# Performance work log

Measured on AMD Instinct MI355X. Metric: run time of the kernel, lower is better.

## Reference

```python
import jax, jax.numpy as jnp
import numpy as np


def setup_inputs() -> dict:
    key = jax.random.key(0)
    kq, kk, kv, km = jax.random.split(key, 4)
    B, H, S, D = 2, 16, 2048, 64
    Q = jax.random.normal(kq, (B, H, S, D), dtype=jnp.float32)
    K = jax.random.normal(kk, (B, H, S, D), dtype=jnp.float32)
    V = jax.random.normal(kv, (B, H, S, D), dtype=jnp.float32)
    mask = jax.random.randint(km, (B, 1, S, S), 0, 2).astype(jnp.bool_)
    return {"Q": Q, "K": K, "V": V, "mask": mask}


def reference(Q, K, V, mask):
    # scores: [B, H, Sq, Sk]
    scores = jnp.einsum("bhqd,bhkd->bhqk", Q, K)
    neg = jnp.finfo(scores.dtype).min
    # Faithful to original: mask fill happens BEFORE the sqrt(d) scaling.
    scores = jnp.where(mask, neg, scores)
    inv_sqrt_d = 1.0 / jnp.sqrt(jnp.asarray(Q.shape[-1], dtype=scores.dtype))
    attn = jax.nn.softmax(scores * inv_sqrt_d, axis=-1)
    return jnp.einsum("bhqk,bhkd->bhqd", attn, V)
```

## Files before the change

kernel.cpp:

```cpp
#include <hip/hip_runtime.h>
#include <stdint.h>


#define SQ 2048
#define DH 64

using bf16x8  = __attribute__((ext_vector_type(8)))  __bf16;
using f32x4   = __attribute__((ext_vector_type(4)))  float;
using ushort8 = __attribute__((ext_vector_type(8)))  unsigned short;
using ushort4v= __attribute__((ext_vector_type(4)))  unsigned short;
using u32x4   = __attribute__((ext_vector_type(4)))  unsigned int;

static __device__ __forceinline__ unsigned short f2bf(float f) {
    union { float f; uint32_t u; } c; c.f = f;
    return (unsigned short)((c.u + 0x8000u) >> 16);
}

static __device__ __forceinline__ uint32_t pkbf(float a, float b) {
    union { __bf16 h[2]; uint32_t u; } t;
    t.h[0] = (__bf16)a; t.h[1] = (__bf16)b;
    return t.u;
}

static __device__ __forceinline__ f32x4 mfma16(bf16x8 a, bf16x8 b, f32x4 c) {
    return __builtin_amdgcn_mfma_f32_16x16x32_bf16(a, b, c, 0, 0, 0);
}

static __device__ __forceinline__ void gload16(const void* g, void* l) {
    __builtin_amdgcn_global_load_lds(
        (const __attribute__((address_space(1))) void*)g,
        (__attribute__((address_space(3))) void*)l, 16, 0, 0);
}

__global__ __launch_bounds__(256)
void prep_kernel(const int* __restrict__ mask, const float* __restrict__ K,
                 const float* __restrict__ V, unsigned long long* __restrict__ words,
                 unsigned short* __restrict__ Kb, unsigned short* __restrict__ Vt) {
    __shared__ unsigned short tl[64][66];
    const int bx  = blockIdx.x;
    const int tid = threadIdx.x;
    if (bx < 32768) {
        int gid = bx * 256 + tid;
        int mv = mask[gid];
        unsigned long long b = __ballot(mv != 0);
        if ((gid & 63) == 0) words[gid >> 6] = b;
    } else if (bx < 36864) {
        int gid = (bx - 32768) * 256 + tid;
        float4 v = ((const float4*)K)[gid];
        ushort4v t;
        t[0]=f2bf(v.x); t[1]=f2bf(v.y); t[2]=f2bf(v.z); t[3]=f2bf(v.w);
        ((ushort4v*)Kb)[gid] = t;
    } else {
        const int vbx = bx - 36864;
        const int kt  = vbx & 31;
        const size_t bh = vbx >> 5;
        const float* vp = V + (bh * SQ + (size_t)kt * 64) * DH;
        #pragma unroll
        for (int i = 0; i < 4; ++i) {
            int idx = tid + 256 * i;
            int key = idx >> 4;
            int dc  = (idx & 15) * 4;
            float4 v = *(const float4*)(vp + (size_t)key * DH + dc);
            tl[key][dc + 0] = f2bf(v.x);
            tl[key][dc + 1] = f2bf(v.y);
            tl[key][dc + 2] = f2bf(v.z);
            tl[key][dc + 3] = f2bf(v.w);
        }
        __syncthreads();
        unsigned short* op = Vt + bh * DH * SQ + (size_t)kt * 64;
        #pragma unroll
        for (int i = 0; i < 4; ++i) {
            int idx = tid + 256 * i;
            int d  = idx >> 4;
            int kc = (idx & 15) * 4;
            ushort4v t;
            t[0] = tl[kc + 0][d]; t[1] = tl[kc + 1][d];
            t[2] = tl[kc + 2][d]; t[3] = tl[kc + 3][d];
            *(ushort4v*)(op + (size_t)d * SQ + kc) = t;
        }
    }
}

__global__ __launch_bounds__(256, 5)
void attn_kernel(const float* __restrict__ Q,
                 const unsigned short* __restrict__ Kb,
                 const unsigned short* __restrict__ Vtg,
                 const unsigned long long* __restrict__ Mw,
                 float* __restrict__ out) {
    __shared__ __align__(16) unsigned short Ks[2][64 * 64];
    __shared__ __align__(16) unsigned short Vs[2][64 * 64];

    const int tid  = threadIdx.x;
    const int w    = tid >> 6;
    const int l    = tid & 63;
    const int quad = l >> 4;
    const int c16  = l & 15;
    const int bx = blockIdx.x;
    const int hh = bx & 15;
    const int b  = (bx >> 4) & 1;
    const int qt = bx >> 5;

    const size_t bh = (size_t)b * 16 + hh;
    const float* Qp = Q + bh * SQ * DH;
    const int qw = qt * 64 + 16 * w;

    const unsigned long long* Mrow = Mw + ((size_t)b * SQ + qw + c16) * (SQ / 64);

    const int s0 = (2 * w) * 64 + l;
    const int s1 = (2 * w + 1) * 64 + l;
    const int r0 = s0 >> 3, g0s = s0 & 7;
    const int r1 = s1 >> 3, g1s = s1 & 7;
    const char* Kg = (const char*)(Kb  + bh * (size_t)SQ * DH);
    const char* Vg = (const char*)(Vtg + bh * (size_t)DH * SQ);
    const char* kSrc0 = Kg + r0 * 128  + ((g0s ^ (r0 & 7)) << 4);
    const char* kSrc1 = Kg + r1 * 128  + ((g1s ^ (r1 & 7)) << 4);
    const char* vSrc0 = Vg + r0 * 4096 + ((g0s ^ (r0 & 7)) << 4);
    const char* vSrc1 = Vg + r1 * 4096 + ((g1s ^ (r1 & 7)) << 4);

    bf16x8 qf[2];
    {
        const float* qr = Qp + (size_t)(qw + c16) * DH;
        #pragma unroll
        for (int c = 0; c < 2; ++c) {
            int d0 = 32 * c + 8 * quad;
            float4 a  = *(const float4*)(qr + d0);
            float4 b4 = *(const float4*)(qr + d0 + 4);
            ushort8 t;
            t[0]=f2bf(a.x);  t[1]=f2bf(a.y);  t[2]=f2bf(a.z);  t[3]=f2bf(a.w);
            t[4]=f2bf(b4.x); t[5]=f2bf(b4.y); t[6]=f2bf(b4.z); t[7]=f2bf(b4.w);
            qf[c] = __builtin_bit_cast(bf16x8, t);
        }
    }

    f32x4 o[4];
    float lsum = 0.f;
    #pragma unroll
    for (int i = 0; i < 4; ++i) o[i] = (f32x4)(0.f);

    const int xg = (c16 & 7);
    int gfrag[2];
    #pragma unroll
    for (int c = 0; c < 2; ++c) gfrag[c] = ((4 * c + quad) ^ xg) << 3;

    const int permA = ((quad & 1) << 1) | (quad >> 1);
    const int addrA = 4 * (c16 + 16 * permA);
    const int addrB = addrA ^ 64;
    const bool oddq = (quad & 1) != 0;

    unsigned long long mw = Mrow[0];

    gload16(kSrc0, &Ks[0][(2 * w) * 512]);
    gload16(kSrc1, &Ks[0][(2 * w + 1) * 512]);
    gload16(vSrc0, &Vs[0][(2 * w) * 512]);
    gload16(vSrc1, &Vs[0][(2 * w + 1) * 512]);
    kSrc0 += 8192; kSrc1 += 8192; vSrc0 += 128; vSrc1 += 128;
    __syncthreads();

    for (int t = 0; t < 32; ++t) {
        const int cur = t & 1;

        unsigned long long nmw = 0;
        if (t < 31) {
            gload16(kSrc0, &Ks[cur ^ 1][(2 * w) * 512]);
            gload16(kSrc1, &Ks[cur ^ 1][(2 * w + 1) * 512]);
            gload16(vSrc0, &Vs[cur ^ 1][(2 * w) * 512]);
            gload16(vSrc1, &Vs[cur ^ 1][(2 * w + 1) * 512]);
            kSrc0 += 8192; kSrc1 += 8192; vSrc0 += 128; vSrc1 += 128;
            nmw = Mrow[t + 1];
        }

        const unsigned short* Kc = Ks[cur];
        const unsigned short* Vc = Vs[cur];

        f32x4 s[4];
        #pragma unroll
        for (int i = 0; i < 4; ++i) s[i] = (f32x4)(0.f);
        __builtin_amdgcn_s_setprio(1);
        #pragma unroll
        for (int c = 0; c < 2; ++c) {
            #pragma unroll
            for (int nb = 0; nb < 4; ++nb) {
                bf16x8 kb = __builtin_bit_cast(bf16x8,
                    *(const ushort8*)&Kc[(c16 + 16 * nb) * 64 + gfrag[c]]);
                s[nb] = mfma16(kb, qf[c], s[nb]);
            }
        }
        __builtin_amdgcn_s_setprio(0);

        const unsigned long long sh = mw >> (4 * quad);
        uint32_t pk[4][2];
        #pragma unroll
        for (int nb = 0; nb < 4; ++nb) {
            float pv[4];
            #pragma unroll
            for (int r = 0; r < 4; ++r) {
                float e = __builtin_amdgcn_exp2f(fmaf(s[nb][r], 0.18033688f, -5.7707802f));
                pv[r] = ((sh >> (16 * nb + r)) & 1ull) ? 0.0f : e;
                lsum += pv[r];
            }
            pk[nb][0] = pkbf(pv[0], pv[1]);
            pk[nb][1] = pkbf(pv[2], pv[3]);
        }

        int sw1_0 = __builtin_amdgcn_ds_swizzle((int)pk[1][0], 0x401F);
        int sw1_1 = __builtin_amdgcn_ds_swizzle((int)pk[1][1], 0x401F);
        int sw3_0 = __builtin_amdgcn_ds_swizzle((int)pk[3][0], 0x401F);
        int sw3_1 = __builtin_amdgcn_ds_swizzle((int)pk[3][1], 0x401F);

        #pragma unroll
        for (int c = 0; c < 2; ++c) {
            const int e0 = (int)pk[2 * c][0];
            const int e1 = (int)pk[2 * c][1];
            const int s0v = c ? sw3_0 : sw1_0;
            const int s1v = c ? sw3_1 : sw1_1;
            u32x4 pw;
            pw[0] = (unsigned)__builtin_amdgcn_ds_bpermute(addrA, oddq ? s0v : e0);
            pw[1] = (unsigned)__builtin_amdgcn_ds_bpermute(addrA, oddq ? s1v : e1);
            pw[2] = (unsigned)__builtin_amdgcn_ds_bpermute(addrB, oddq ? e0 : s0v);
            pw[3] = (unsigned)__builtin_amdgcn_ds_bpermute(addrB, oddq ? e1 : s1v);
            bf16x8 pa = __builtin_bit_cast(bf16x8, pw);

            __builtin_amdgcn_s_setprio(1);
            #pragma unroll
            for (int db = 0; db < 4; ++db) {
                bf16x8 vb = __builtin_bit_cast(bf16x8,
                    *(const ushort8*)&Vc[(c16 + 16 * db) * 64 + gfrag[c]]);
                o[db] = mfma16(vb, pa, o[db]);
            }
            __builtin_amdgcn_s_setprio(0);
        }

        __syncthreads();
        mw = nmw;
    }

    float v = lsum;
    v += __shfl_xor(v, 16, 64);
    v += __shfl_xor(v, 32, 64);
    const float rinv = 1.0f / v;
    float* op = out + (bh * SQ + (size_t)(qw + c16)) * DH + 4 * quad;
    #pragma unroll
    for (int db = 0; db < 4; ++db) {
        float4 st;
        st.x = o[db][0] * rinv; st.y = o[db][1] * rinv;
        st.z = o[db][2] * rinv; st.w = o[db][3] * rinv;
        *(float4*)(op + 16 * db) = st;
    }
}

extern "C" void kernel_launch(void* const* d_in, const int* in_sizes, int n_in,
                              void* d_out, int out_size, void* d_ws, size_t ws_size,
                              hipStream_t stream) {
    const float* Q    = (const float*)d_in[0];
    const float* K    = (const float*)d_in[1];
    const float* V    = (const float*)d_in[2];
    const int*   mask = (const int*)d_in[3];
    float* out = (float*)d_out;

    char* ws = (char*)d_ws;
    unsigned long long* mwords = (unsigned long long*)ws;
    unsigned short* Kb = (unsigned short*)(ws + (1 << 20));
    unsigned short* Vt = (unsigned short*)(ws + (1 << 20) + (8 << 20));

    prep_kernel<<<dim3(37888), dim3(256), 0, stream>>>(mask, K, V, mwords, Kb, Vt);
    attn_kernel<<<dim3(1024), dim3(256), 0, stream>>>(Q, Kb, Vt, mwords, out);
}
```

Baseline: 191.1 us.

## Use two-wave blocks with 32 query rows per wave and LDS P transpose

Attention blocks shrink from four waves to two, and each wave now handles two 16-row query subtiles. Each K/V fragment read from LDS therefore feeds two MFMAs, which halves LDS reads per MFMA. The P-matrix relayout switches from ds_swizzle/bpermute to a per-wave LDS staging buffer. The cost is higher register pressure (double accumulators, launch bounds 128,2) and fewer waves per block to hide latency.

```diff
diff --git a/kernel.cpp b/kernel.cpp
--- a/kernel.cpp
+++ b/kernel.cpp
@@ -9,7 +9,6 @@
 using f32x4   = __attribute__((ext_vector_type(4)))  float;
 using ushort8 = __attribute__((ext_vector_type(8)))  unsigned short;
 using ushort4v= __attribute__((ext_vector_type(4)))  unsigned short;
-using u32x4   = __attribute__((ext_vector_type(4)))  unsigned int;
 
 static __device__ __forceinline__ unsigned short f2bf(float f) {
     union { float f; uint32_t u; } c; c.f = f;
@@ -81,7 +80,7 @@
     }
 }
 
-__global__ __launch_bounds__(256, 5)
+__global__ __launch_bounds__(128, 2)
 void attn_kernel(const float* __restrict__ Q,
                  const unsigned short* __restrict__ Kb,
                  const unsigned short* __restrict__ Vtg,
@@ -89,6 +88,7 @@
                  float* __restrict__ out) {
     __shared__ __align__(16) unsigned short Ks[2][64 * 64];
     __shared__ __align__(16) unsigned short Vs[2][64 * 64];
+    __shared__ __align__(16) unsigned short Ps[2 * 16 * 64];
 
     const int tid  = threadIdx.x;
     const int w    = tid >> 6;
@@ -102,24 +102,28 @@
 
     const size_t bh = (size_t)b * 16 + hh;
     const float* Qp = Q + bh * SQ * DH;
-    const int qw = qt * 64 + 16 * w;
-
-    const unsigned long long* Mrow = Mw + ((size_t)b * SQ + qw + c16) * (SQ / 64);
-
-    const int s0 = (2 * w) * 64 + l;
-    const int s1 = (2 * w + 1) * 64 + l;
-    const int r0 = s0 >> 3, g0s = s0 & 7;
-    const int r1 = s1 >> 3, g1s = s1 & 7;
+    const int qw = qt * 64 + 32 * w;
+
+    const unsigned long long* Mrow0 = Mw + ((size_t)b * SQ + qw + c16) * (SQ / 64);
+    const unsigned long long* Mrow1 = Mrow0 + 16 * (SQ / 64);
+
+    const int lr = l >> 3;
+    const int gg = l & 7;
+    const int off16 = ((gg ^ lr) << 4);
     const char* Kg = (const char*)(Kb  + bh * (size_t)SQ * DH);
     const char* Vg = (const char*)(Vtg + bh * (size_t)DH * SQ);
-    const char* kSrc0 = Kg + r0 * 128  + ((g0s ^ (r0 & 7)) << 4);
-    const char* kSrc1 = Kg + r1 * 128  + ((g1s ^ (r1 & 7)) << 4);
-    const char* vSrc0 = Vg + r0 * 4096 + ((g0s ^ (r0 & 7)) << 4);
-    const char* vSrc1 = Vg + r1 * 4096 + ((g1s ^ (r1 & 7)) << 4);
-
-    bf16x8 qf[2];
-    {
-        const float* qr = Qp + (size_t)(qw + c16) * DH;
+    const char* kS[4]; const char* vS[4];
+    #pragma unroll
+    for (int i = 0; i < 4; ++i) {
+        int row = 32 * w + 8 * i + lr;
+        kS[i] = Kg + (size_t)row * 128  + off16;
+        vS[i] = Vg + (size_t)row * 4096 + off16;
+    }
+
+    bf16x8 qf[2][2];
+    #pragma unroll
+    for (int sub = 0; sub < 2; ++sub) {
+        const float* qr = Qp + (size_t)(qw + 16 * sub + c16) * DH;
         #pragma unroll
         for (int c = 0; c < 2; ++c) {
             int d0 = 32 * c + 8 * quad;
@@ -128,53 +132,57 @@
             ushort8 t;
             t[0]=f2bf(a.x);  t[1]=f2bf(a.y);  t[2]=f2bf(a.z);  t[3]=f2bf(a.w);
             t[4]=f2bf(b4.x); t[5]=f2bf(b4.y); t[6]=f2bf(b4.z); t[7]=f2bf(b4.w);
-            qf[c] = __builtin_bit_cast(bf16x8, t);
-        }
-    }
-
-    f32x4 o[4];
-    float lsum = 0.f;
-    #pragma unroll
-    for (int i = 0; i < 4; ++i) o[i] = (f32x4)(0.f);
-
+            qf[sub][c] = __builtin_bit_cast(bf16x8, t);
+        }
+    }
+
+    f32x4 o0[4], o1[4];
+    float lsum0 = 0.f, lsum1 = 0.f;
+    #pragma unroll
+    for (int i = 0; i < 4; ++i) { o0[i] = (f32x4)(0.f); o1[i] = (f32x4)(0.f); }
+
+    unsigned short* Pw = Ps + w * (16 * 64);
     const int xg = (c16 & 7);
     int gfrag[2];
     #pragma unroll
     for (int c = 0; c < 2; ++c) gfrag[c] = ((4 * c + quad) ^ xg) << 3;
-
-    const int permA = ((quad & 1) << 1) | (quad >> 1);
-    const int addrA = 4 * (c16 + 16 * permA);
-    const int addrB = addrA ^ 64;
-    const bool oddq = (quad & 1) != 0;
-
-    unsigned long long mw = Mrow[0];
-
-    gload16(kSrc0, &Ks[0][(2 * w) * 512]);
-    gload16(kSrc1, &Ks[0][(2 * w + 1) * 512]);
-    gload16(vSrc0, &Vs[0][(2 * w) * 512]);
-    gload16(vSrc1, &Vs[0][(2 * w + 1) * 512]);
-    kSrc0 += 8192; kSrc1 += 8192; vSrc0 += 128; vSrc1 += 128;
+    int poff[4];
+    #pragma unroll
+    for (int nb = 0; nb < 4; ++nb)
+        poff[nb] = c16 * 64 + (((2 * nb + (quad >> 1)) ^ xg) << 3) + 4 * (quad & 1);
+    const int paoff0 = c16 * 64 + gfrag[0];
+    const int paoff1 = c16 * 64 + gfrag[1];
+
+    unsigned long long mw0 = Mrow0[0], mw1 = Mrow1[0];
+    #pragma unroll
+    for (int i = 0; i < 4; ++i) {
+        gload16(kS[i], &Ks[0][(4 * w + i) * 512]);
+        gload16(vS[i], &Vs[0][(4 * w + i) * 512]);
+        kS[i] += 8192; vS[i] += 128;
+    }
     __syncthreads();
 
     for (int t = 0; t < 32; ++t) {
         const int cur = t & 1;
 
-        unsigned long long nmw = 0;
+        unsigned long long nmw0 = 0, nmw1 = 0;
         if (t < 31) {
-            gload16(kSrc0, &Ks[cur ^ 1][(2 * w) * 512]);
-            gload16(kSrc1, &Ks[cur ^ 1][(2 * w + 1) * 512]);
-            gload16(vSrc0, &Vs[cur ^ 1][(2 * w) * 512]);
-            gload16(vSrc1, &Vs[cur ^ 1][(2 * w + 1) * 512]);
-            kSrc0 += 8192; kSrc1 += 8192; vSrc0 += 128; vSrc1 += 128;
-            nmw = Mrow[t + 1];
+            #pragma unroll
+            for (int i = 0; i < 4; ++i) {
+                gload16(kS[i], &Ks[cur ^ 1][(4 * w + i) * 512]);
+                gload16(vS[i], &Vs[cur ^ 1][(4 * w + i) * 512]);
+                kS[i] += 8192; vS[i] += 128;
+            }
+            nmw0 = Mrow0[t + 1];
+            nmw1 = Mrow1[t + 1];
         }
 
         const unsigned short* Kc = Ks[cur];
         const unsigned short* Vc = Vs[cur];
 
-        f32x4 s[4];
-        #pragma unroll
-        for (int i = 0; i < 4; ++i) s[i] = (f32x4)(0.f);
+        f32x4 s0[4], s1[4];
+        #pragma unroll
+        for (int i = 0; i < 4; ++i) { s0[i] = (f32x4)(0.f); s1[i] = (f32x4)(0.f); }
         __builtin_amdgcn_s_setprio(1);
         #pragma unroll
         for (int c = 0; c < 2; ++c) {
@@ -182,69 +190,103 @@
             for (int nb = 0; nb < 4; ++nb) {
                 bf16x8 kb = __builtin_bit_cast(bf16x8,
                     *(const ushort8*)&Kc[(c16 + 16 * nb) * 64 + gfrag[c]]);
-                s[nb] = mfma16(kb, qf[c], s[nb]);
+                s0[nb] = mfma16(kb, qf[0][c], s0[nb]);
+                s1[nb] = mfma16(kb, qf[1][c], s1[nb]);
             }
         }
         __builtin_amdgcn_s_setprio(0);
 
-        const unsigned long long sh = mw >> (4 * quad);
-        uint32_t pk[4][2];
+        uint32_t pk0[4][2], pk1[4][2];
+        {
+            const unsigned long long sh = mw0 >> (4 * quad);
+            #pragma unroll
+            for (int nb = 0; nb < 4; ++nb) {
+                float pv[4];
+                #pragma unroll
+                for (int r = 0; r < 4; ++r) {
+                    float e = __builtin_amdgcn_exp2f(fmaf(s0[nb][r], 0.18033688f, -5.7707802f));
+                    pv[r] = ((sh >> (16 * nb + r)) & 1ull) ? 0.0f : e;
+                    lsum0 += pv[r];
+                }
+                pk0[nb][0] = pkbf(pv[0], pv[1]);
+                pk0[nb][1] = pkbf(pv[2], pv[3]);
+            }
+            #pragma unroll
+            for (int nb = 0; nb < 4; ++nb) {
+                uint2 wv; wv.x = pk0[nb][0]; wv.y = pk0[nb][1];
+                *(uint2*)&Pw[poff[nb]] = wv;
+            }
+        }
+        {
+            const unsigned long long sh = mw1 >> (4 * quad);
+            #pragma unroll
+            for (int nb = 0; nb < 4; ++nb) {
+                float pv[4];
+                #pragma unroll
+                for (int r = 0; r < 4; ++r) {
+                    float e = __builtin_amdgcn_exp2f(fmaf(s1[nb][r], 0.18033688f, -5.7707802f));
+                    pv[r] = ((sh >> (16 * nb + r)) & 1ull) ? 0.0f : e;
+                    lsum1 += pv[r];
+                }
+                pk1[nb][0] = pkbf(pv[0], pv[1]);
+                pk1[nb][1] = pkbf(pv[2], pv[3]);
+            }
+        }
+        bf16x8 pa0[2], pa1[2];
+        pa0[0] = __builtin_bit_cast(bf16x8, *(const ushort8*)&Pw[paoff0]);
+        pa0[1] = __builtin_bit_cast(bf16x8, *(const ushort8*)&Pw[paoff1]);
         #pragma unroll
         for (int nb = 0; nb < 4; ++nb) {
-            float pv[4];
-            #pragma unroll
-            for (int r = 0; r < 4; ++r) {
-                float e = __builtin_amdgcn_exp2f(fmaf(s[nb][r], 0.18033688f, -5.7707802f));
-                pv[r] = ((sh >> (16 * nb + r)) & 1ull) ? 0.0f : e;
-                lsum += pv[r];
-            }
-            pk[nb][0] = pkbf(pv[0], pv[1]);
-            pk[nb][1] = pkbf(pv[2], pv[3]);
-        }
-
-        int sw1_0 = __builtin_amdgcn_ds_swizzle((int)pk[1][0], 0x401F);
-        int sw1_1 = __builtin_amdgcn_ds_swizzle((int)pk[1][1], 0x401F);
-        int sw3_0 = __builtin_amdgcn_ds_swizzle((int)pk[3][0], 0x401F);
-        int sw3_1 = __builtin_amdgcn_ds_swizzle((int)pk[3][1], 0x401F);
-
+            uint2 wv; wv.x = pk1[nb][0]; wv.y = pk1[nb][1];
+            *(uint2*)&Pw[poff[nb]] = wv;
+        }
+        pa1[0] = __builtin_bit_cast(bf16x8, *(const ushort8*)&Pw[paoff0]);
+        pa1[1] = __builtin_bit_cast(bf16x8, *(const ushort8*)&Pw[paoff1]);
+
+        __builtin_amdgcn_s_setprio(1);
         #pragma unroll
         for (int c = 0; c < 2; ++c) {
-            const int e0 = (int)pk[2 * c][0];
-            const int e1 = (int)pk[2 * c][1];
-            const int s0v = c ? sw3_0 : sw1_0;
-            const int s1v = c ? sw3_1 : sw1_1;
-            u32x4 pw;
-            pw[0] = (unsigned)__builtin_amdgcn_ds_bpermute(addrA, oddq ? s0v : e0);
-            pw[1] = (unsigned)__builtin_amdgcn_ds_bpermute(addrA, oddq ? s1v : e1);
-            pw[2] = (unsigned)__builtin_amdgcn_ds_bpermute(addrB, oddq ? e0 : s0v);
-            pw[3] = (unsigned)__builtin_amdgcn_ds_bpermute(addrB, oddq ? e1 : s1v);
-            bf16x8 pa = __builtin_bit_cast(bf16x8, pw);
-
-            __builtin_amdgcn_s_setprio(1);
             #pragma unroll
             for (int db = 0; db < 4; ++db) {
                 bf16x8 vb = __builtin_bit_cast(bf16x8,
                     *(const ushort8*)&Vc[(c16 + 16 * db) * 64 + gfrag[c]]);
-                o[db] = mfma16(vb, pa, o[db]);
-            }
-            __builtin_amdgcn_s_setprio(0);
-        }
+                o0[db] = mfma16(vb, pa0[c], o0[db]);
+                o1[db] = mfma16(vb, pa1[c], o1[db]);
+            }
+        }
+        __builtin_amdgcn_s_setprio(0);
 
         __syncthreads();
-        mw = nmw;
-    }
-
-    float v = lsum;
-    v += __shfl_xor(v, 16, 64);
-    v += __shfl_xor(v, 32, 64);
-    const float rinv = 1.0f / v;
-    float* op = out + (bh * SQ + (size_t)(qw + c16)) * DH + 4 * quad;
-    #pragma unroll
-    for (int db = 0; db < 4; ++db) {
-        float4 st;
-        st.x = o[db][0] * rinv; st.y = o[db][1] * rinv;
-        st.z = o[db][2] * rinv; st.w = o[db][3] * rinv;
-        *(float4*)(op + 16 * db) = st;
+        mw0 = nmw0; mw1 = nmw1;
+    }
+
+    {
+        float v = lsum0;
+        v += __shfl_xor(v, 16, 64);
+        v += __shfl_xor(v, 32, 64);
+        const float rinv = 1.0f / v;
+        float* op = out + (bh * SQ + (size_t)(qw + c16)) * DH + 4 * quad;
+        #pragma unroll
+        for (int db = 0; db < 4; ++db) {
+            float4 st;
+            st.x = o0[db][0] * rinv; st.y = o0[db][1] * rinv;
+            st.z = o0[db][2] * rinv; st.w = o0[db][3] * rinv;
+            *(float4*)(op + 16 * db) = st;
+        }
+    }
+    {
+        float v = lsum1;
+        v += __shfl_xor(v, 16, 64);
+        v += __shfl_xor(v, 32, 64);
+        const float rinv = 1.0f / v;
+        float* op = out + (bh * SQ + (size_t)(qw + 16 + c16)) * DH + 4 * quad;
+        #pragma unroll
+        for (int db = 0; db < 4; ++db) {
+            float4 st;
+            st.x = o1[db][0] * rinv; st.y = o1[db][1] * rinv;
+            st.z = o1[db][2] * rinv; st.w = o1[db][3] * rinv;
+            *(float4*)(op + 16 * db) = st;
+        }
     }
 }
 
@@ -263,5 +305,5 @@
     unsigned short* Vt = (unsigned short*)(ws + (1 << 20) + (8 << 20));
 
     prep_kernel<<<dim3(37888), dim3(256), 0, stream>>>(mask, K, V, mwords, Kb, Vt);
-    attn_kernel<<<dim3(1024), dim3(256), 0, stream>>>(Q, Kb, Vt, mwords, out);
-}
+    attn_kernel<<<dim3(1024), dim3(128), 0, stream>>>(Q, Kb, Vt, mwords, out);
+}
```

New measurement: 190.8 us. No clear change (-0.1%).

## Permute V-transpose key order to drop cross-lane P shuffles in attention

Applied to the files above, without the earlier changes.

The V transpose prep kernel now writes keys in a permuted order within each 64-key tile, so the register layout of the softmax probabilities already matches the MFMA A-operand. This removes the ds_swizzle and ds_bpermute shuffles that moved P between lanes before the PV matmul, and groups the PV MFMAs under one priority region. Launch bounds are also relaxed from 5 to 4 waves per SIMD, which gives the compiler more registers but may lower occupancy.

```diff
diff --git a/kernel.cpp b/kernel.cpp
--- a/kernel.cpp
+++ b/kernel.cpp
@@ -72,16 +72,18 @@
         for (int i = 0; i < 4; ++i) {
             int idx = tid + 256 * i;
             int d  = idx >> 4;
-            int kc = (idx & 15) * 4;
+            int m  = idx & 15;
+            int kc = m * 4;
+            int pos = 32 * (m >> 3) + 8 * (m & 3) + 4 * ((m >> 2) & 1);
             ushort4v t;
             t[0] = tl[kc + 0][d]; t[1] = tl[kc + 1][d];
             t[2] = tl[kc + 2][d]; t[3] = tl[kc + 3][d];
-            *(ushort4v*)(op + (size_t)d * SQ + kc) = t;
-        }
-    }
-}
-
-__global__ __launch_bounds__(256, 5)
+            *(ushort4v*)(op + (size_t)d * SQ + pos) = t;
+        }
+    }
+}
+
+__global__ __launch_bounds__(256, 4)
 void attn_kernel(const float* __restrict__ Q,
                  const unsigned short* __restrict__ Kb,
                  const unsigned short* __restrict__ Vtg,
@@ -142,13 +144,7 @@
     #pragma unroll
     for (int c = 0; c < 2; ++c) gfrag[c] = ((4 * c + quad) ^ xg) << 3;
 
-    const int permA = ((quad & 1) << 1) | (quad >> 1);
-    const int addrA = 4 * (c16 + 16 * permA);
-    const int addrB = addrA ^ 64;
-    const bool oddq = (quad & 1) != 0;
-
     unsigned long long mw = Mrow[0];
-
     gload16(kSrc0, &Ks[0][(2 * w) * 512]);
     gload16(kSrc1, &Ks[0][(2 * w + 1) * 512]);
     gload16(vSrc0, &Vs[0][(2 * w) * 512]);
@@ -187,48 +183,43 @@
         }
         __builtin_amdgcn_s_setprio(0);
 
-        const unsigned long long sh = mw >> (4 * quad);
         uint32_t pk[4][2];
-        #pragma unroll
-        for (int nb = 0; nb < 4; ++nb) {
-            float pv[4];
+        {
+            const unsigned long long sh = mw >> (4 * quad);
             #pragma unroll
-            for (int r = 0; r < 4; ++r) {
-                float e = __builtin_amdgcn_exp2f(fmaf(s[nb][r], 0.18033688f, -5.7707802f));
-                pv[r] = ((sh >> (16 * nb + r)) & 1ull) ? 0.0f : e;
-                lsum += pv[r];
+            for (int nb = 0; nb < 4; ++nb) {
+                float pv[4];
+                #pragma unroll
+                for (int r = 0; r < 4; ++r) {
+                    float e = __builtin_amdgcn_exp2f(fmaf(s[nb][r], 0.18033688f, -5.7707802f));
+                    pv[r] = ((sh >> (16 * nb + r)) & 1ull) ? 0.0f : e;
+                    lsum += pv[r];
+                }
+                pk[nb][0] = pkbf(pv[0], pv[1]);
+                pk[nb][1] = pkbf(pv[2], pv[3]);
             }
-            pk[nb][0] = pkbf(pv[0], pv[1]);
-            pk[nb][1] = pkbf(pv[2], pv[3]);
-        }
-
-        int sw1_0 = __builtin_amdgcn_ds_swizzle((int)pk[1][0], 0x401F);
-        int sw1_1 = __builtin_amdgcn_ds_swizzle((int)pk[1][1], 0x401F);
-        int sw3_0 = __builtin_amdgcn_ds_swizzle((int)pk[3][0], 0x401F);
-        int sw3_1 = __builtin_amdgcn_ds_swizzle((int)pk[3][1], 0x401F);
-
-        #pragma unroll
-        for (int c = 0; c < 2; ++c) {
-            const int e0 = (int)pk[2 * c][0];
-            const int e1 = (int)pk[2 * c][1];
-            const int s0v = c ? sw3_0 : sw1_0;
-            const int s1v = c ? sw3_1 : sw1_1;
-            u32x4 pw;
-            pw[0] = (unsigned)__builtin_amdgcn_ds_bpermute(addrA, oddq ? s0v : e0);
-            pw[1] = (unsigned)__builtin_amdgcn_ds_bpermute(addrA, oddq ? s1v : e1);
-            pw[2] = (unsigned)__builtin_amdgcn_ds_bpermute(addrB, oddq ? e0 : s0v);
-            pw[3] = (unsigned)__builtin_amdgcn_ds_bpermute(addrB, oddq ? e1 : s1v);
-            bf16x8 pa = __builtin_bit_cast(bf16x8, pw);
-
-            __builtin_amdgcn_s_setprio(1);
+        }
+
+        bf16x8 pa[2];
+        #pragma unroll
+        for (int c = 0; c < 2; ++c) {
+            u32x4 tv;
+            tv[0] = pk[2 * c][0];     tv[1] = pk[2 * c][1];
+            tv[2] = pk[2 * c + 1][0]; tv[3] = pk[2 * c + 1][1];
+            pa[c] = __builtin_bit_cast(bf16x8, tv);
+        }
+
+        __builtin_amdgcn_s_setprio(1);
+        #pragma unroll
+        for (int c = 0; c < 2; ++c) {
             #pragma unroll
             for (int db = 0; db < 4; ++db) {
                 bf16x8 vb = __builtin_bit_cast(bf16x8,
                     *(const ushort8*)&Vc[(c16 + 16 * db) * 64 + gfrag[c]]);
-                o[db] = mfma16(vb, pa, o[db]);
+                o[db] = mfma16(vb, pa[c], o[db]);
             }
-            __builtin_amdgcn_s_setprio(0);
-        }
+        }
+        __builtin_amdgcn_s_setprio(0);
 
         __syncthreads();
         mw = nmw;
```

Result: faster. 186.2 us (-2.6%).
